# Performance work log

Measured on AMD Instinct MI355X. Metric: run time of the kernel, lower is better.

Reference implementation:

```python
import jax, jax.numpy as jnp
import numpy as np

CELL = 512
DENSE = 2048
PRED = 24 * 24  # predict_ahead * 24
FEAT = 24
FORGET_BIAS = 1.0


def setup_inputs() -> dict:
    key = jax.random.key(0)
    ks = jax.random.split(key, 7)
    B, T = 1024, 512
    s = lambda fan_in: 1.0 / np.sqrt(fan_in)
    return {
        "X": jax.random.normal(ks[0], (B, T, FEAT), dtype=jnp.float32),
        "W_lstm": jax.random.normal(ks[1], (FEAT + CELL, 4 * CELL), dtype=jnp.float32) * s(FEAT + CELL),
        "b_lstm": jnp.zeros((4 * CELL,), dtype=jnp.float32),
        "W_dense": jax.random.normal(ks[2], (CELL, DENSE), dtype=jnp.float32) * s(CELL),
        "b_dense": jnp.zeros((DENSE,), dtype=jnp.float32),
        "W_pred": jax.random.normal(ks[3], (DENSE, PRED), dtype=jnp.float32) * s(DENSE),
        "b_pred": jnp.zeros((PRED,), dtype=jnp.float32),
    }


def reference(X, W_lstm, b_lstm, W_dense, b_dense, W_pred, b_pred):
    B = X.shape[0]
    c0 = jnp.zeros((B, CELL), dtype=X.dtype)
    h0 = jnp.zeros((B, CELL), dtype=X.dtype)

    def step(carry, x_t):
        c, h = carry
        z = jnp.concatenate([x_t, h], axis=1) @ W_lstm + b_lstm  # [B, 4*CELL]
        i, j, f, o = jnp.split(z, 4, axis=1)  # TF BasicLSTMCell gate order
        new_c = c * jax.nn.sigmoid(f + FORGET_BIAS) + jax.nn.sigmoid(i) * jnp.tanh(j)
        new_h = jnp.tanh(new_c) * jax.nn.sigmoid(o)
        return (new_c, new_h), None

    xs = jnp.swapaxes(X, 0, 1)  # [T, B, FEAT]
    (c_T, h_T), _ = jax.lax.scan(step, (c0, h0), xs)
    dense = jax.nn.relu(h_T @ W_dense + b_dense)
    preds = dense @ W_pred + b_pred
    return preds
```

## Files before the change

kernel.cpp:

```cpp
#include <hip/hip_runtime.h>
#include <hip/hip_fp16.h>

#define BATCH 1024
#define SEQ 512
#define NFEAT 24
#define NCELL 512
#define ZC 2048
#define KP 544
#define NCH 17
#define KL 576
#define DENSE_N 2048
#define PRED_N 576
#define NWG 256
#define NGRP 8
#define GWG 32
#define PFD 4
#define NBUF 5

typedef unsigned short u16;
typedef unsigned int u32;
typedef unsigned long long u64;
typedef unsigned short u16x8 __attribute__((ext_vector_type(8)));
typedef _Float16 f16x8 __attribute__((ext_vector_type(8)));
typedef float f32x4 __attribute__((ext_vector_type(4)));

__device__ __forceinline__ float sigm(float x) { return 1.f / (1.f + __expf(-x)); }
__device__ __forceinline__ float ftanh(float x) {
    float t = __expf(-2.f * fabsf(x));
    float r = (1.f - t) / (1.f + t);
    return copysignf(r, x);
}
__device__ __forceinline__ u16 f2h(float v) {
    _Float16 h = (_Float16)v;
    return *(u16*)&h;
}
__device__ __forceinline__ void st16(u16* p, u32 v) {
    asm volatile("global_store_short %0, %1, off sc0 sc1" :: "v"(p), "v"(v) : "memory");
}
__device__ __forceinline__ void st128(u16* p, u16x8 v) {
    asm volatile("global_store_dwordx4 %0, %1, off sc0 sc1" :: "v"(p), "v"(v) : "memory");
}

__device__ __forceinline__ u32 hword16(int row, int k) {
    int rb = row >> 7, wv = (row >> 5) & 3, m = (row >> 4) & 1;
    int ch = k >> 5;
    int lane = (row & 15) | (((k >> 3) & 3) << 4);
    return (u32)((((rb * 4 + wv) * NCH + ch) * 2 + m) * 512 + lane * 8 + (k & 7));
}

__global__ __launch_bounds__(256) void prep_w(const float* __restrict__ W,
                                              u16* __restrict__ Wt) {
    int o = blockIdx.x * 256 + threadIdx.x;
    if (o >= ZC * KP) return;
    int n = o / KP, k = o % KP;
    float v = 0.f;
    if (k < NCELL)              v = W[(size_t)(NFEAT + k) * ZC + n];
    else if (k < NCELL + NFEAT) v = W[(size_t)(k - NCELL) * ZC + n];
    Wt[o] = f2h(v);
}

__global__ __launch_bounds__(256) void prep_h(const float* __restrict__ X,
                                              u16* __restrict__ H0, u16* __restrict__ H1) {
    int o = blockIdx.x * 256 + threadIdx.x;
    if (o >= BATCH * KP) return;
    int row = o / KP, k = o % KP;
    u16 b = 0;
    if (k >= NCELL && k < NCELL + NFEAT)
        b = f2h(X[(size_t)row * (SEQ * NFEAT) + (k - NCELL)]);
    u32 w = hword16(row, k);
    H0[w] = b;
    H1[w] = 0;
}

__global__ __launch_bounds__(256, 1) void lstm_persist(
    u16* __restrict__ H0, u16* __restrict__ H1,
    const u16* __restrict__ Wt,
    const float* __restrict__ bias,
    const float* __restrict__ X,
    float* __restrict__ hf32,
    int* __restrict__ bar)
{
    extern __shared__ u16 Ws[];

    const int tid = (int)threadIdx.x;
    const int bid = (int)blockIdx.x;
    const int rb = bid & 7, nb = bid >> 3;
    const int r0 = rb * 128;
    const int lane = tid & 63, wv = tid >> 6;
    u16* __restrict__ Hs = Ws + 64 * KL;
    int* __restrict__ bcnt   = bar + rb * 64;
    int* __restrict__ bepoch = bar + rb * 64 + 32;

    for (int e = tid; e < 64 * (KP / 8); e += 256) {
        int col = e / (KP / 8), k8 = (e % (KP / 8)) * 8;
        int zc = (col >> 4) * NCELL + nb * 16 + (col & 15);
        int so = k8 ^ ((col & 7) << 3);
        *(u16x8*)&Ws[col * KL + so] = *(const u16x8*)&Wt[(size_t)zc * KP + k8];
    }
    __syncthreads();

    const int cell = nb * 16 + (lane & 15);
    const float bi = bias[cell], bj = bias[NCELL + cell];
    const float bf_ = bias[2 * NCELL + cell], bo = bias[3 * NCELL + cell];

    const int akof = (lane >> 4) * 8;
    const u32 abase0 = (u32)(((rb * 4 + wv) * NCH) * 2 + 0) * 128u + (u32)lane * 2u;
    const u32 abase1 = abase0 + 128u;

    const int esub2 = (nb & 1) * 2;
    const u32 efrag = (u32)((rb * 4 + wv) * NCH + (nb >> 1)) * 2u;
    const u32 esto = ((efrag + (u32)(lane >> 5)) << 9)
                   + (u32)((esub2 * 16 + (lane & 31)) << 3);
    const int hsw = (wv << 9);

    float ct[2][4] = {};

    for (int t = 0; t < SEQ; ++t) {
        const u64* Hq = (const u64*)((t & 1) ? H1 : H0);
        u16*       Np = (t & 1) ? H0 : H1;

        f32x4 acc[2][4] = {};
        __attribute__((aligned(16))) u64 fr[NBUF][4];

#define ALOADS(f, ch) do { \
        f[0] = __hip_atomic_load(&Hq[abase0 + (u32)(ch) * 256u],     __ATOMIC_RELAXED, __HIP_MEMORY_SCOPE_AGENT); \
        f[1] = __hip_atomic_load(&Hq[abase0 + (u32)(ch) * 256u + 1], __ATOMIC_RELAXED, __HIP_MEMORY_SCOPE_AGENT); \
        f[2] = __hip_atomic_load(&Hq[abase1 + (u32)(ch) * 256u],     __ATOMIC_RELAXED, __HIP_MEMORY_SCOPE_AGENT); \
        f[3] = __hip_atomic_load(&Hq[abase1 + (u32)(ch) * 256u + 1], __ATOMIC_RELAXED, __HIP_MEMORY_SCOPE_AGENT); \
        } while (0)
#define WSOFF(cb, off) ((cb) * KL + (((off)) ^ (((cb) & 7) << 3)))
#define CCOMP(f, ch) do { \
        f16x8 a0 = *(const f16x8*)&f[0]; \
        f16x8 a1 = *(const f16x8*)&f[2]; \
        _Pragma("unroll") \
        for (int n = 0; n < 4; ++n) { \
            f16x8 bn = *(const f16x8*)&Ws[WSOFF(n * 16 + (lane & 15), (ch) * 32 + akof)]; \
            acc[0][n] = __builtin_amdgcn_mfma_f32_16x16x32_f16(a0, bn, acc[0][n], 0, 0, 0); \
            acc[1][n] = __builtin_amdgcn_mfma_f32_16x16x32_f16(a1, bn, acc[1][n], 0, 0, 0); \
        } } while (0)

        ALOADS(fr[0], 0); ALOADS(fr[1], 1); ALOADS(fr[2], 2); ALOADS(fr[3], 3);
        #pragma unroll
        for (int ch = 0; ch < NCH; ++ch) {
            if (ch + PFD < NCH) ALOADS(fr[(ch + PFD) % NBUF], ch + PFD);
            CCOMP(fr[ch % NBUF], ch);
        }
#undef ALOADS
#undef CCOMP

        #pragma unroll
        for (int m = 0; m < 2; ++m) {
            #pragma unroll
            for (int r = 0; r < 4; ++r) {
                int row16 = (lane >> 4) * 4 + r;
                float zi = acc[m][0][r] + bi;
                float zj = acc[m][1][r] + bj;
                float zf = acc[m][2][r] + bf_;
                float zo = acc[m][3][r] + bo;
                float cn = ct[m][r] * sigm(zf + 1.0f) + sigm(zi) * ftanh(zj);
                ct[m][r] = cn;
                float h = ftanh(cn) * sigm(zo);
                Hs[hsw + (m << 8) + (((lane >> 3) & 1) << 7) + (row16 << 3) + (lane & 7)] = f2h(h);
                if (t == SEQ - 1) {
                    int row = r0 + wv * 32 + m * 16 + row16;
                    hf32[(size_t)row * NCELL + cell] = h;
                }
            }
        }
        {
            u16x8 v = *(const u16x8*)&Hs[hsw + lane * 8];
            st128(&Np[esto], v);
        }
        if (t + 1 < SEQ && nb < NFEAT && tid < 128) {
            int row = r0 + tid;
            float v = X[(size_t)row * (SEQ * NFEAT) + (t + 1) * NFEAT + nb];
            int wv2 = tid >> 5, m2 = (tid >> 4) & 1;
            int elane2 = (tid & 15) | ((nb >> 3) << 4);
            u32 idx = (u32)(((rb * 4 + wv2) * NCH + 16) * 2 + m2) * 512u
                    + (u32)(elane2 * 8 + (nb & 7));
            st16(&Np[idx], (u32)f2h(v));
        }

        __syncthreads();
        if (tid == 0) {
            int n = __hip_atomic_fetch_add(bcnt, 1, __ATOMIC_RELAXED, __HIP_MEMORY_SCOPE_AGENT);
            if (n == GWG - 1) {
                __hip_atomic_store(bcnt, 0, __ATOMIC_RELAXED, __HIP_MEMORY_SCOPE_AGENT);
                __hip_atomic_store(bepoch, t + 1, __ATOMIC_RELAXED, __HIP_MEMORY_SCOPE_AGENT);
            } else {
                int spins = 0;
                while (__hip_atomic_load(bepoch, __ATOMIC_RELAXED, __HIP_MEMORY_SCOPE_AGENT) <= t) {
                    __builtin_amdgcn_s_sleep(4);
                    if (++spins > 20000000) break;
                }
            }
        }
        __syncthreads();
    }
}

template <int ACT>
__global__ __launch_bounds__(256) void gemm64(
    const float* __restrict__ A, const float* __restrict__ Wm,
    const float* __restrict__ bias, float* __restrict__ out,
    int M, int N, int K)
{
    __shared__ float Asf[32][65];
    __shared__ float Bsf[32][65];
    const int c0 = blockIdx.x * 64;
    const int r0 = blockIdx.y * 64;
    const int tid = (int)threadIdx.x;
    const int tx = tid & 15, ty = tid >> 4;

    float acc[4][4];
    #pragma unroll
    for (int r = 0; r < 4; ++r) { acc[r][0]=0.f; acc[r][1]=0.f; acc[r][2]=0.f; acc[r][3]=0.f; }

    for (int k0 = 0; k0 < K; k0 += 32) {
        #pragma unroll
        for (int i = 0; i < 8; ++i) {
            int e = tid + 256 * i;
            int row = e >> 5, kk = e & 31;
            Asf[kk][row] = A[(size_t)(r0 + row) * K + k0 + kk];
        }
        #pragma unroll
        for (int i = 0; i < 8; ++i) {
            int e = tid + 256 * i;
            int kk = e >> 6, cl = e & 63;
            Bsf[kk][cl] = Wm[(size_t)(k0 + kk) * N + c0 + cl];
        }
        __syncthreads();
        #pragma unroll
        for (int kk = 0; kk < 32; ++kk) {
            float b0 = Bsf[kk][tx*4], b1 = Bsf[kk][tx*4+1], b2 = Bsf[kk][tx*4+2], b3 = Bsf[kk][tx*4+3];
            #pragma unroll
            for (int r = 0; r < 4; ++r) {
                float a = Asf[kk][ty*4 + r];
                acc[r][0] = fmaf(a, b0, acc[r][0]);
                acc[r][1] = fmaf(a, b1, acc[r][1]);
                acc[r][2] = fmaf(a, b2, acc[r][2]);
                acc[r][3] = fmaf(a, b3, acc[r][3]);
            }
        }
        __syncthreads();
    }
    #pragma unroll
    for (int r = 0; r < 4; ++r) {
        int gr = r0 + ty * 4 + r;
        #pragma unroll
        for (int j = 0; j < 4; ++j) {
            int gc = c0 + tx * 4 + j;
            float v = acc[r][j] + bias[gc];
            if (ACT) v = fmaxf(v, 0.f);
            out[(size_t)gr * N + gc] = v;
        }
    }
}

extern "C" void kernel_launch(void* const* d_in, const int* in_sizes, int n_in,
                              void* d_out, int out_size, void* d_ws, size_t ws_size,
                              hipStream_t stream)
{
    const float* X  = (const float*)d_in[0];
    const float* Wl = (const float*)d_in[1];
    const float* bl = (const float*)d_in[2];
    const float* Wd = (const float*)d_in[3];
    const float* bd = (const float*)d_in[4];
    const float* Wp = (const float*)d_in[5];
    const float* bp = (const float*)d_in[6];
    float* out = (float*)d_out;

    char* p = (char*)d_ws;
    int* bar      = (int*)p; p += 4096;
    float* hf32   = (float*)p; p += (size_t)BATCH * NCELL * 4;
    float* dense  = (float*)p; p += (size_t)BATCH * DENSE_N * 4;
    u16* Wt   = (u16*)p; p += (size_t)ZC * KP * 2;
    u16* H0   = (u16*)p; p += (size_t)BATCH * KP * 2;
    u16* H1   = (u16*)p; p += (size_t)BATCH * KP * 2;

    (void)hipMemsetAsync(bar, 0, 4096, stream);
    prep_w<<<(ZC * KP) / 256, 256, 0, stream>>>(Wl, Wt);
    prep_h<<<(BATCH * KP) / 256, 256, 0, stream>>>(X, H0, H1);

    const int lds_bytes = 64 * KL * 2 + 4 * 512 * 2;
    (void)hipFuncSetAttribute((const void*)lstm_persist,
                              hipFuncAttributeMaxDynamicSharedMemorySize, lds_bytes);
    lstm_persist<<<NWG, 256, lds_bytes, stream>>>(H0, H1, Wt, bl, X, hf32, bar);

    dim3 blk(256);
    gemm64<1><<<dim3(DENSE_N / 64, BATCH / 64), blk, 0, stream>>>(hf32, Wd, bd, dense, BATCH, DENSE_N, NCELL);
    gemm64<0><<<dim3(PRED_N / 64, BATCH / 64), blk, 0, stream>>>(dense, Wp, bp, out, BATCH, PRED_N, DENSE_N);
}
```

Measured before the change: 3.190 ms.

## Retile persistent LSTM into 16 row groups of 64 with 32 cells per block

Changes the persistent LSTM decomposition from 8 row groups of 128 rows × 16 cells to 16 row groups of 64 rows × 32 cells. Each block now holds twice the recurrent weights in LDS and reads half as many h rows per step. Each grid barrier group shrinks from 32 to 16 workgroups, cutting global h traffic per block and barrier contention. It also deepens the load prefetch and shortens the spin sleep. The trade-off is a larger LDS footprint and a rewritten h/X layout that must stay consistent with prep_h.

```diff
diff --git a/kernel.cpp b/kernel.cpp
--- a/kernel.cpp
+++ b/kernel.cpp
@@ -12,10 +12,10 @@
 #define DENSE_N 2048
 #define PRED_N 576
 #define NWG 256
-#define NGRP 8
-#define GWG 32
-#define PFD 4
-#define NBUF 5
+#define NGRP 16
+#define GWG 16
+#define PFD 6
+#define NBUF 7
 
 typedef unsigned short u16;
 typedef unsigned int u32;
@@ -42,10 +42,10 @@
 }
 
 __device__ __forceinline__ u32 hword16(int row, int k) {
-    int rb = row >> 7, wv = (row >> 5) & 3, m = (row >> 4) & 1;
-    int ch = k >> 5;
-    int lane = (row & 15) | (((k >> 3) & 3) << 4);
-    return (u32)((((rb * 4 + wv) * NCH + ch) * 2 + m) * 512 + lane * 8 + (k & 7));
+    int g = row >> 6, w = (row >> 4) & 3, r = row & 15;
+    int ch = k >> 5, kk = k & 31;
+    return (u32)(((g * 4 + w) * NCH + ch) * 512)
+         + (u32)(((r | ((kk >> 3) << 4)) << 3) + (kk & 7));
 }
 
 __global__ __launch_bounds__(256) void prep_w(const float* __restrict__ W,
@@ -84,33 +84,33 @@
 
     const int tid = (int)threadIdx.x;
     const int bid = (int)blockIdx.x;
-    const int rb = bid & 7, nb = bid >> 3;
-    const int r0 = rb * 128;
+    const int g = bid & 15, nb2 = bid >> 4;
+    const int r0 = g * 64;
     const int lane = tid & 63, wv = tid >> 6;
-    u16* __restrict__ Hs = Ws + 64 * KL;
-    int* __restrict__ bcnt   = bar + rb * 64;
-    int* __restrict__ bepoch = bar + rb * 64 + 32;
-
-    for (int e = tid; e < 64 * (KP / 8); e += 256) {
+    u16* __restrict__ Hs = Ws + 128 * KL;
+    int* __restrict__ bcnt   = bar + g * 64;
+    int* __restrict__ bepoch = bar + g * 64 + 32;
+
+    for (int e = tid; e < 128 * (KP / 8); e += 256) {
         int col = e / (KP / 8), k8 = (e % (KP / 8)) * 8;
-        int zc = (col >> 4) * NCELL + nb * 16 + (col & 15);
+        int n = col >> 4, cl = col & 15;
+        int zc = (n & 3) * NCELL + nb2 * 32 + (n >> 2) * 16 + cl;
         int so = k8 ^ ((col & 7) << 3);
         *(u16x8*)&Ws[col * KL + so] = *(const u16x8*)&Wt[(size_t)zc * KP + k8];
     }
     __syncthreads();
 
-    const int cell = nb * 16 + (lane & 15);
-    const float bi = bias[cell], bj = bias[NCELL + cell];
-    const float bf_ = bias[2 * NCELL + cell], bo = bias[3 * NCELL + cell];
+    const int cell0 = nb2 * 32 + (lane & 15);
+    const int cell1 = cell0 + 16;
+    const float bi0 = bias[cell0],           bi1 = bias[cell1];
+    const float bj0 = bias[NCELL + cell0],   bj1 = bias[NCELL + cell1];
+    const float bf0 = bias[2*NCELL + cell0], bf1 = bias[2*NCELL + cell1];
+    const float bo0 = bias[3*NCELL + cell0], bo1 = bias[3*NCELL + cell1];
 
     const int akof = (lane >> 4) * 8;
-    const u32 abase0 = (u32)(((rb * 4 + wv) * NCH) * 2 + 0) * 128u + (u32)lane * 2u;
-    const u32 abase1 = abase0 + 128u;
-
-    const int esub2 = (nb & 1) * 2;
-    const u32 efrag = (u32)((rb * 4 + wv) * NCH + (nb >> 1)) * 2u;
-    const u32 esto = ((efrag + (u32)(lane >> 5)) << 9)
-                   + (u32)((esub2 * 16 + (lane & 31)) << 3);
+    const u32 abase = (u32)((g * 4 + wv) * NCH) * 128u + (u32)lane * 2u;
+
+    const u32 esto = (u32)((g * 4 + wv) * NCH + nb2) * 512u + (u32)lane * 8u;
     const int hsw = (wv << 9);
 
     float ct[2][4] = {};
@@ -119,27 +119,24 @@
         const u64* Hq = (const u64*)((t & 1) ? H1 : H0);
         u16*       Np = (t & 1) ? H0 : H1;
 
-        f32x4 acc[2][4] = {};
-        __attribute__((aligned(16))) u64 fr[NBUF][4];
+        f32x4 acc[8] = {};
+        __attribute__((aligned(16))) u64 fr[NBUF][2];
 
 #define ALOADS(f, ch) do { \
-        f[0] = __hip_atomic_load(&Hq[abase0 + (u32)(ch) * 256u],     __ATOMIC_RELAXED, __HIP_MEMORY_SCOPE_AGENT); \
-        f[1] = __hip_atomic_load(&Hq[abase0 + (u32)(ch) * 256u + 1], __ATOMIC_RELAXED, __HIP_MEMORY_SCOPE_AGENT); \
-        f[2] = __hip_atomic_load(&Hq[abase1 + (u32)(ch) * 256u],     __ATOMIC_RELAXED, __HIP_MEMORY_SCOPE_AGENT); \
-        f[3] = __hip_atomic_load(&Hq[abase1 + (u32)(ch) * 256u + 1], __ATOMIC_RELAXED, __HIP_MEMORY_SCOPE_AGENT); \
+        f[0] = __hip_atomic_load(&Hq[abase + (u32)(ch) * 128u],     __ATOMIC_RELAXED, __HIP_MEMORY_SCOPE_AGENT); \
+        f[1] = __hip_atomic_load(&Hq[abase + (u32)(ch) * 128u + 1], __ATOMIC_RELAXED, __HIP_MEMORY_SCOPE_AGENT); \
         } while (0)
 #define WSOFF(cb, off) ((cb) * KL + (((off)) ^ (((cb) & 7) << 3)))
 #define CCOMP(f, ch) do { \
-        f16x8 a0 = *(const f16x8*)&f[0]; \
-        f16x8 a1 = *(const f16x8*)&f[2]; \
+        f16x8 a = *(const f16x8*)&f[0]; \
         _Pragma("unroll") \
-        for (int n = 0; n < 4; ++n) { \
+        for (int n = 0; n < 8; ++n) { \
             f16x8 bn = *(const f16x8*)&Ws[WSOFF(n * 16 + (lane & 15), (ch) * 32 + akof)]; \
-            acc[0][n] = __builtin_amdgcn_mfma_f32_16x16x32_f16(a0, bn, acc[0][n], 0, 0, 0); \
-            acc[1][n] = __builtin_amdgcn_mfma_f32_16x16x32_f16(a1, bn, acc[1][n], 0, 0, 0); \
+            acc[n] = __builtin_amdgcn_mfma_f32_16x16x32_f16(a, bn, acc[n], 0, 0, 0); \
         } } while (0)
 
-        ALOADS(fr[0], 0); ALOADS(fr[1], 1); ALOADS(fr[2], 2); ALOADS(fr[3], 3);
+        ALOADS(fr[0], 0); ALOADS(fr[1], 1); ALOADS(fr[2], 2);
+        ALOADS(fr[3], 3); ALOADS(fr[4], 4); ALOADS(fr[5], 5);
         #pragma unroll
         for (int ch = 0; ch < NCH; ++ch) {
             if (ch + PFD < NCH) ALOADS(fr[(ch + PFD) % NBUF], ch + PFD);
@@ -149,21 +146,21 @@
 #undef CCOMP
 
         #pragma unroll
-        for (int m = 0; m < 2; ++m) {
+        for (int c2 = 0; c2 < 2; ++c2) {
             #pragma unroll
             for (int r = 0; r < 4; ++r) {
                 int row16 = (lane >> 4) * 4 + r;
-                float zi = acc[m][0][r] + bi;
-                float zj = acc[m][1][r] + bj;
-                float zf = acc[m][2][r] + bf_;
-                float zo = acc[m][3][r] + bo;
-                float cn = ct[m][r] * sigm(zf + 1.0f) + sigm(zi) * ftanh(zj);
-                ct[m][r] = cn;
+                float zi = acc[c2 * 4 + 0][r] + (c2 ? bi1 : bi0);
+                float zj = acc[c2 * 4 + 1][r] + (c2 ? bj1 : bj0);
+                float zf = acc[c2 * 4 + 2][r] + (c2 ? bf1 : bf0);
+                float zo = acc[c2 * 4 + 3][r] + (c2 ? bo1 : bo0);
+                float cn = ct[c2][r] * sigm(zf + 1.0f) + sigm(zi) * ftanh(zj);
+                ct[c2][r] = cn;
                 float h = ftanh(cn) * sigm(zo);
-                Hs[hsw + (m << 8) + (((lane >> 3) & 1) << 7) + (row16 << 3) + (lane & 7)] = f2h(h);
+                Hs[hsw + ((row16 | ((c2 * 2 + ((lane >> 3) & 1)) << 4)) << 3) + (lane & 7)] = f2h(h);
                 if (t == SEQ - 1) {
-                    int row = r0 + wv * 32 + m * 16 + row16;
-                    hf32[(size_t)row * NCELL + cell] = h;
+                    int row = r0 + wv * 16 + row16;
+                    hf32[(size_t)row * NCELL + (c2 ? cell1 : cell0)] = h;
                 }
             }
         }
@@ -171,13 +168,14 @@
             u16x8 v = *(const u16x8*)&Hs[hsw + lane * 8];
             st128(&Np[esto], v);
         }
-        if (t + 1 < SEQ && nb < NFEAT && tid < 128) {
-            int row = r0 + tid;
-            float v = X[(size_t)row * (SEQ * NFEAT) + (t + 1) * NFEAT + nb];
-            int wv2 = tid >> 5, m2 = (tid >> 4) & 1;
-            int elane2 = (tid & 15) | ((nb >> 3) << 4);
-            u32 idx = (u32)(((rb * 4 + wv2) * NCH + 16) * 2 + m2) * 512u
-                    + (u32)(elane2 * 8 + (nb & 7));
+        if (t + 1 < SEQ && tid < 96) {
+            int e = nb2 * 96 + tid;
+            int rowg = e / 24, kk = e % 24;
+            int row = r0 + rowg;
+            float v = X[(size_t)row * (SEQ * NFEAT) + (t + 1) * NFEAT + kk];
+            int w2 = rowg >> 4, r16 = rowg & 15;
+            u32 idx = (u32)((g * 4 + w2) * NCH + 16) * 512u
+                    + (u32)(((r16 | ((kk >> 3) << 4)) << 3) + (kk & 7));
             st16(&Np[idx], (u32)f2h(v));
         }
 
@@ -190,7 +188,7 @@
             } else {
                 int spins = 0;
                 while (__hip_atomic_load(bepoch, __ATOMIC_RELAXED, __HIP_MEMORY_SCOPE_AGENT) <= t) {
-                    __builtin_amdgcn_s_sleep(4);
+                    __builtin_amdgcn_s_sleep(2);
                     if (++spins > 20000000) break;
                 }
             }
@@ -282,7 +280,7 @@
     prep_w<<<(ZC * KP) / 256, 256, 0, stream>>>(Wl, Wt);
     prep_h<<<(BATCH * KP) / 256, 256, 0, stream>>>(X, H0, H1);
 
-    const int lds_bytes = 64 * KL * 2 + 4 * 512 * 2;
+    const int lds_bytes = 128 * KL * 2 + 4 * 512 * 2;
     (void)hipFuncSetAttribute((const void*)lstm_persist,
                               hipFuncAttributeMaxDynamicSharedMemorySize, lds_bytes);
     lstm_persist<<<NWG, 256, lds_bytes, stream>>>(H0, H1, Wt, bl, X, hf32, bar);
```

Result: faster. 2.911 ms (-8.7%).
